# Kernel tuning notes

Hardware: AMD Instinct MI355X
Metric: run time of the kernel (lower is better)

Reference implementation:

```python
import jax, jax.numpy as jnp
import numpy as np

B, N, DH = 8, 2048, 512
EPS = 1e-5


def _layer_norm(x, g, b):
    m = x.mean(-1, keepdims=True)
    v = ((x - m) ** 2).mean(-1, keepdims=True)
    return (x - m) * jax.lax.rsqrt(v + EPS) * g + b


def setup_inputs() -> dict:
    key = jax.random.key(0)
    ks = jax.random.split(key, 20)
    s = 1.0 / np.sqrt(DH)
    sf = 1.0 / np.sqrt(2 * DH)
    return {
        "H": jax.random.normal(ks[0], (B, N, DH), jnp.float32),
        "adj": jax.random.uniform(ks[1], (B, N, N), jnp.float32),
        "hop_emb": jax.random.normal(ks[2], (N, DH), jnp.float32),
        "Wq": jax.random.normal(ks[3], (DH, DH), jnp.float32) * s,
        "bq": jnp.zeros((DH,), jnp.float32),
        "Wk": jax.random.normal(ks[4], (DH, DH), jnp.float32) * s,
        "bk": jnp.zeros((DH,), jnp.float32),
        "Wv": jax.random.normal(ks[5], (DH, DH), jnp.float32) * s,
        "bv": jnp.zeros((DH,), jnp.float32),
        "W1": jax.random.normal(ks[6], (DH, 2 * DH), jnp.float32) * s,
        "b1": jnp.zeros((2 * DH,), jnp.float32),
        "W2": jax.random.normal(ks[7], (2 * DH, DH), jnp.float32) * sf,
        "b2": jnp.zeros((DH,), jnp.float32),
        "g1": jnp.ones((DH,), jnp.float32),
        "be1": jnp.zeros((DH,), jnp.float32),
        "g2": jnp.ones((DH,), jnp.float32),
        "be2": jnp.zeros((DH,), jnp.float32),
    }


def reference(H, adj, hop_emb, Wq, bq, Wk, bk, Wv, bv, W1, b1, W2, b2, g1, be1, g2, be2):
    Q = H @ Wq + bq                                     # [B,N,DH]
    K = H @ Wk + bk
    V = H @ Wv + bv
    scores = jnp.einsum("bid,bjd->bij", Q, K) / np.sqrt(DH).astype(np.float32)
    # (adj[...,None] * hop_emb).mean(-1) == adj * hop_emb.mean(-1)[j]
    hop_effect = adj * hop_emb.mean(-1)[None, None, :]  # [B,N,N]
    attn = jax.nn.softmax(scores * hop_effect, axis=-1)
    attn_out = jnp.einsum("bij,bjd->bid", attn, V)
    x = _layer_norm(attn_out + H, g1, be1)
    ffn = jax.nn.relu(x @ W1 + b1) @ W2 + b2
    return _layer_norm(ffn + x, g2, be2)
```

## Files before the change

kernel.cpp:

```cpp
#include <hip/hip_runtime.h>

typedef unsigned short u16;
typedef __bf16 bf16x8 __attribute__((ext_vector_type(8)));
typedef float f32x4 __attribute__((ext_vector_type(4)));

#define SEQN 2048
#define DHID 512

static __device__ __forceinline__ float bf2f(u16 u) {
    union { unsigned int i; float f; } c; c.i = ((unsigned int)u) << 16; return c.f;
}
static __device__ __forceinline__ u16 f2bf(float f) {
    union { float f; unsigned int i; } c; c.f = f;
    unsigned int x = c.i;
    return (u16)((x + 0x7fffu + ((x >> 16) & 1u)) >> 16);
}

static __device__ __forceinline__ void gld_lds16(const u16* g, u16* l) {
    __builtin_amdgcn_global_load_lds(
        (__attribute__((address_space(1))) void*)(g),
        (__attribute__((address_space(3))) void*)(l), 16, 0, 0);
}

__global__ __launch_bounds__(256) void cvt_kernel(const float* __restrict__ src,
                                                  u16* __restrict__ dst, int n) {
    int i = (blockIdx.x * 256 + threadIdx.x) * 8;
    if (i >= n) return;
    float4 a = *(const float4*)(src + i);
    float4 b = *(const float4*)(src + i + 4);
    union { uint4 u; u16 s[8]; } o;
    o.s[0] = f2bf(a.x); o.s[1] = f2bf(a.y); o.s[2] = f2bf(a.z); o.s[3] = f2bf(a.w);
    o.s[4] = f2bf(b.x); o.s[5] = f2bf(b.y); o.s[6] = f2bf(b.z); o.s[7] = f2bf(b.w);
    *(uint4*)(dst + i) = o.u;
}

__global__ __launch_bounds__(256) void cvt_t_kernel(const float* __restrict__ src,
                                                    u16* __restrict__ dst, int K, int N) {
    int idx = blockIdx.x * 256 + threadIdx.x;
    if (idx >= K * N) return;
    int n = idx / K, k = idx - n * K;
    dst[idx] = f2bf(src[(size_t)k * N + n]);
}

__global__ void hmean_kernel(const float* __restrict__ hop, float* __restrict__ hm) {
    int j = blockIdx.x, t = threadIdx.x;
    const float* p = hop + (size_t)j * DHID + t * 8;
    float4 a = *(const float4*)p;
    float4 b = *(const float4*)(p + 4);
    float s = a.x + a.y + a.z + a.w + b.x + b.y + b.z + b.w;
#pragma unroll
    for (int m = 1; m < 64; m <<= 1) s += __shfl_xor(s, m);
    if (t == 0) hm[j] = s * (1.0f / (float)DHID);
}

enum { EPI_BIAS = 0, EPI_RELU = 1, EPI_PLAIN = 3, EPI_BIAS_T = 4, EPI_QKV = 5 };

template <int EPI>
__global__ __launch_bounds__(256) void gemm_bt(
    const u16* __restrict__ A, const u16* __restrict__ Bt, u16* __restrict__ C,
    const float* __restrict__ bias,
    int K, int lda, int ldb, int ldc,
    u16* __restrict__ Qo, u16* __restrict__ Ko, u16* __restrict__ Vto,
    const float* __restrict__ bq_, const float* __restrict__ bk_,
    const float* __restrict__ bv_)
{
    __shared__ u16 As[128 * 32];
    __shared__ u16 Bs[128 * 32];

    const int tid = threadIdx.x;
    const u16* Ab = A;
    const u16* Bb = Bt;

    const int bm0 = blockIdx.y * 128, bn0 = blockIdx.x * 128;
    const int wid = tid >> 6, lane = tid & 63, quad = lane >> 4, l16 = lane & 15;
    const int wm = (wid >> 1) * 64, wn = (wid & 1) * 64;
    const int srow = lane >> 2;
    const int skof = (lane & 3) * 8;

    f32x4 acc[4][4];
#pragma unroll
    for (int i = 0; i < 4; ++i)
#pragma unroll
        for (int j = 0; j < 4; ++j) acc[i][j] = (f32x4){0.f, 0.f, 0.f, 0.f};

    for (int k0 = 0; k0 < K; k0 += 32) {
#pragma unroll
        for (int it = 0; it < 2; ++it) {
            int c = wid * 2 + it;
            gld_lds16(Ab + (size_t)(bm0 + c * 16 + srow) * lda + k0 + skof,
                      &As[c * 512]);
        }
#pragma unroll
        for (int it = 0; it < 2; ++it) {
            int c = wid * 2 + it;
            gld_lds16(Bb + (size_t)(bn0 + c * 16 + srow) * ldb + k0 + skof,
                      &Bs[c * 512]);
        }
        __syncthreads();

        bf16x8 af[4], bfr[4];
#pragma unroll
        for (int i = 0; i < 4; ++i)
            af[i] = *(const bf16x8*)&As[(wm + i * 16 + l16) * 32 + quad * 8];
#pragma unroll
        for (int j = 0; j < 4; ++j)
            bfr[j] = *(const bf16x8*)&Bs[(wn + j * 16 + l16) * 32 + quad * 8];
#pragma unroll
        for (int i = 0; i < 4; ++i)
#pragma unroll
            for (int j = 0; j < 4; ++j)
                acc[i][j] = __builtin_amdgcn_mfma_f32_16x16x32_bf16(af[i], bfr[j], acc[i][j], 0, 0, 0);
        __syncthreads();
    }

#pragma unroll
    for (int i = 0; i < 4; ++i) {
#pragma unroll
        for (int j = 0; j < 4; ++j) {
            const int gn = bn0 + wn + j * 16 + l16;
            const int gm0 = bm0 + wm + i * 16 + quad * 4;
            if constexpr (EPI == EPI_BIAS || EPI == EPI_RELU) {
                const float b = bias[gn];
#pragma unroll
                for (int r = 0; r < 4; ++r) {
                    float v = acc[i][j][r] + b;
                    if constexpr (EPI == EPI_RELU) v = fmaxf(v, 0.f);
                    C[(size_t)(gm0 + r) * ldc + gn] = f2bf(v);
                }
            } else if constexpr (EPI == EPI_BIAS_T) {
                const float b = bias[gn];
                const int bb = gm0 >> 11, n = gm0 & 2047;
                ushort4 o;
                o.x = f2bf(acc[i][j][0] + b);
                o.y = f2bf(acc[i][j][1] + b);
                o.z = f2bf(acc[i][j][2] + b);
                o.w = f2bf(acc[i][j][3] + b);
                *(ushort4*)&C[((size_t)bb * 512 + gn) * 2048 + n] = o;
            } else if constexpr (EPI == EPI_QKV) {
                const int sel = gn >> 9;
                const int n = gn & 511;
                if (sel == 0) {
                    const float b = bq_[n];
#pragma unroll
                    for (int r = 0; r < 4; ++r)
                        Qo[(size_t)(gm0 + r) * DHID + n] = f2bf(acc[i][j][r] + b);
                } else if (sel == 1) {
                    const float b = bk_[n];
#pragma unroll
                    for (int r = 0; r < 4; ++r)
                        Ko[(size_t)(gm0 + r) * DHID + n] = f2bf(acc[i][j][r] + b);
                } else {
                    const float b = bv_[n];
                    const int bb = gm0 >> 11, nn2 = gm0 & 2047;
                    ushort4 o;
                    o.x = f2bf(acc[i][j][0] + b);
                    o.y = f2bf(acc[i][j][1] + b);
                    o.z = f2bf(acc[i][j][2] + b);
                    o.w = f2bf(acc[i][j][3] + b);
                    *(ushort4*)&Vto[((size_t)bb * 512 + n) * 2048 + nn2] = o;
                }
            } else {
#pragma unroll
                for (int r = 0; r < 4; ++r)
                    C[(size_t)(gm0 + r) * ldc + gn] = f2bf(acc[i][j][r]);
            }
        }
    }
}

__global__ __launch_bounds__(256, 2) void attn_kernel(
    const u16* __restrict__ Q, const u16* __restrict__ K, const u16* __restrict__ Vt,
    const float* __restrict__ adj, const float* __restrict__ hm,
    u16* __restrict__ AO)
{
    extern __shared__ u16 lds[];
    u16* Ks = lds;
    u16* Vs = lds + 16384;

    const int tid = threadIdx.x, wid = tid >> 6, lane = tid & 63;
    const int quad = lane >> 4, l16 = lane & 15;
    const int b = blockIdx.x;
    const int q0 = blockIdx.y * 32 + (wid >> 1) * 16;
    const int D0 = (wid & 1) * 256;
    const int srow = lane >> 2, sko = (lane & 3) * 8;

    const u16* Qg = Q + (size_t)b * SEQN * DHID;
    const u16* Kg = K + (size_t)b * SEQN * DHID;
    const u16* Vg = Vt + (size_t)b * DHID * SEQN;
    const float* adjg = adj + (size_t)b * SEQN * SEQN;
    u16* AOg = AO + (size_t)b * SEQN * DHID;
    u16* Plds = lds + wid * 640;

    const float scale = 0.044194173824159216f;

    bf16x8 qf[16];
#pragma unroll
    for (int ds = 0; ds < 16; ++ds)
        qf[ds] = *(const bf16x8*)(Qg + (size_t)(q0 + l16) * DHID + ds * 32 + quad * 8);

    f32x4 oacc[16];
#pragma unroll
    for (int dt = 0; dt < 16; ++dt) oacc[dt] = (f32x4){0.f, 0.f, 0.f, 0.f};
    float lsum[4] = {0.f, 0.f, 0.f, 0.f};

    for (int kt = 0; kt < 64; ++kt) {
        const int kv0 = kt * 32;

#pragma unroll
        for (int i = 0; i < 8; ++i) {
            int id = wid * 8 + i;
            int ds = id >> 1, c = id & 1;
            gld_lds16(Kg + (size_t)(kv0 + c * 16 + srow) * DHID + ds * 32 + sko,
                      &Ks[ds * 1024 + c * 512]);
        }
        __syncthreads();

#pragma unroll
        for (int i = 0; i < 8; ++i) {
            int id = wid * 8 + i;
            gld_lds16(Vg + (size_t)(id * 16 + srow) * SEQN + kv0 + sko,
                      &Vs[id * 512]);
        }

        float hv0 = hm[kv0 + l16] * scale;
        float hv1 = hm[kv0 + 16 + l16] * scale;
        float av[8];
        const float* arow = adjg + (size_t)(q0 + quad * 4) * SEQN + kv0;
#pragma unroll
        for (int r = 0; r < 4; ++r) {
            av[r]     = arow[(size_t)r * SEQN + l16];
            av[4 + r] = arow[(size_t)r * SEQN + 16 + l16];
        }

        f32x4 s0a = {0.f,0.f,0.f,0.f}, s0b = {0.f,0.f,0.f,0.f};
        f32x4 s1a = {0.f,0.f,0.f,0.f}, s1b = {0.f,0.f,0.f,0.f};
#pragma unroll
        for (int ds = 0; ds < 16; ds += 2) {
            bf16x8 k00 = *(const bf16x8*)&Ks[ds * 1024 + l16 * 32 + quad * 8];
            bf16x8 k01 = *(const bf16x8*)&Ks[ds * 1024 + 512 + l16 * 32 + quad * 8];
            s0a = __builtin_amdgcn_mfma_f32_16x16x32_bf16(qf[ds], k00, s0a, 0, 0, 0);
            s1a = __builtin_amdgcn_mfma_f32_16x16x32_bf16(qf[ds], k01, s1a, 0, 0, 0);
            bf16x8 k10 = *(const bf16x8*)&Ks[(ds + 1) * 1024 + l16 * 32 + quad * 8];
            bf16x8 k11 = *(const bf16x8*)&Ks[(ds + 1) * 1024 + 512 + l16 * 32 + quad * 8];
            s0b = __builtin_amdgcn_mfma_f32_16x16x32_bf16(qf[ds + 1], k10, s0b, 0, 0, 0);
            s1b = __builtin_amdgcn_mfma_f32_16x16x32_bf16(qf[ds + 1], k11, s1b, 0, 0, 0);
        }
        f32x4 s0 = s0a + s0b, s1 = s1a + s1b;
        __syncthreads();

#pragma unroll
        for (int r = 0; r < 4; ++r) {
            float p0 = __expf(s0[r] * av[r] * hv0);
            float p1 = __expf(s1[r] * av[4 + r] * hv1);
            lsum[r] += p0 + p1;
            Plds[(quad * 4 + r) * 40 + l16] = f2bf(p0);
            Plds[(quad * 4 + r) * 40 + 16 + l16] = f2bf(p1);
        }
        asm volatile("s_waitcnt lgkmcnt(0)" ::: "memory");

        bf16x8 pf = *(const bf16x8*)&Plds[l16 * 40 + quad * 8];
#pragma unroll
        for (int dt = 0; dt < 16; ++dt) {
            bf16x8 vf = *(const bf16x8*)&Vs[(D0 + dt * 16 + l16) * 32 + quad * 8];
            oacc[dt] = __builtin_amdgcn_mfma_f32_16x16x32_bf16(pf, vf, oacc[dt], 0, 0, 0);
        }
        __syncthreads();
    }

#pragma unroll
    for (int r = 0; r < 4; ++r) {
#pragma unroll
        for (int m = 1; m < 16; m <<= 1) lsum[r] += __shfl_xor(lsum[r], m);
        lsum[r] = 1.f / lsum[r];
    }
#pragma unroll
    for (int dt = 0; dt < 16; ++dt) {
#pragma unroll
        for (int r = 0; r < 4; ++r) {
            AOg[(size_t)(q0 + quad * 4 + r) * DHID + D0 + dt * 16 + l16] =
                f2bf(oacc[dt][r] * lsum[r]);
        }
    }
}

__global__ __launch_bounds__(256) void ln_hf32_kernel(
    const u16* __restrict__ a, const float* __restrict__ Hf,
    const float* __restrict__ g, const float* __restrict__ be,
    u16* __restrict__ out)
{
    size_t row = blockIdx.x;
    int t = threadIdx.x, wid = t >> 6, lane = t & 63;
    unsigned int va = *(const unsigned int*)(a + row * (size_t)DHID + t * 2);
    float2 h = *(const float2*)(Hf + row * (size_t)DHID + t * 2);
    float x0 = bf2f((u16)(va & 0xffff)) + h.x;
    float x1 = bf2f((u16)(va >> 16)) + h.y;
    float s = x0 + x1, sq = x0 * x0 + x1 * x1;
#pragma unroll
    for (int m = 1; m < 64; m <<= 1) { s += __shfl_xor(s, m); sq += __shfl_xor(sq, m); }
    __shared__ float rs[4], rq[4];
    if (lane == 0) { rs[wid] = s; rq[wid] = sq; }
    __syncthreads();
    s = rs[0] + rs[1] + rs[2] + rs[3];
    sq = rq[0] + rq[1] + rq[2] + rq[3];
    float mean = s * (1.f / (float)DHID);
    float var = sq * (1.f / (float)DHID) - mean * mean;
    float rstd = rsqrtf(var + 1e-5f);
    float2 vg = *(const float2*)(g + t * 2);
    float2 vbe = *(const float2*)(be + t * 2);
    float y0 = (x0 - mean) * rstd * vg.x + vbe.x;
    float y1 = (x1 - mean) * rstd * vg.y + vbe.y;
    unsigned int o = (unsigned int)f2bf(y0) | ((unsigned int)f2bf(y1) << 16);
    *(unsigned int*)(out + row * (size_t)DHID + t * 2) = o;
}

__global__ __launch_bounds__(256) void ln_kernel_f32out(
    const u16* __restrict__ a, const u16* __restrict__ bp,
    const float* __restrict__ g, const float* __restrict__ be,
    float* __restrict__ out)
{
    size_t row = blockIdx.x;
    int t = threadIdx.x, wid = t >> 6, lane = t & 63;
    unsigned int va = *(const unsigned int*)(a + row * (size_t)DHID + t * 2);
    unsigned int vb = *(const unsigned int*)(bp + row * (size_t)DHID + t * 2);
    float x0 = bf2f((u16)(va & 0xffff)) + bf2f((u16)(vb & 0xffff));
    float x1 = bf2f((u16)(va >> 16)) + bf2f((u16)(vb >> 16));
    float s = x0 + x1, sq = x0 * x0 + x1 * x1;
#pragma unroll
    for (int m = 1; m < 64; m <<= 1) { s += __shfl_xor(s, m); sq += __shfl_xor(sq, m); }
    __shared__ float rs[4], rq[4];
    if (lane == 0) { rs[wid] = s; rq[wid] = sq; }
    __syncthreads();
    s = rs[0] + rs[1] + rs[2] + rs[3];
    sq = rq[0] + rq[1] + rq[2] + rq[3];
    float mean = s * (1.f / (float)DHID);
    float var = sq * (1.f / (float)DHID) - mean * mean;
    float rstd = rsqrtf(var + 1e-5f);
    float2 vg = *(const float2*)(g + t * 2);
    float2 vbe = *(const float2*)(be + t * 2);
    float y0 = (x0 - mean) * rstd * vg.x + vbe.x;
    float y1 = (x1 - mean) * rstd * vg.y + vbe.y;
    *(float2*)(out + row * (size_t)DHID + t * 2) = make_float2(y0, y1);
}

extern "C" void kernel_launch(void* const* d_in, const int* in_sizes, int n_in,
                              void* d_out, int out_size, void* d_ws, size_t ws_size,
                              hipStream_t stream) {
    const float* H   = (const float*)d_in[0];
    const float* adj = (const float*)d_in[1];
    const float* hop = (const float*)d_in[2];
    const float* Wq  = (const float*)d_in[3];
    const float* bq  = (const float*)d_in[4];
    const float* Wk  = (const float*)d_in[5];
    const float* bk  = (const float*)d_in[6];
    const float* Wv  = (const float*)d_in[7];
    const float* bv  = (const float*)d_in[8];
    const float* W1  = (const float*)d_in[9];
    const float* b1  = (const float*)d_in[10];
    const float* W2  = (const float*)d_in[11];
    const float* b2  = (const float*)d_in[12];
    const float* g1  = (const float*)d_in[13];
    const float* be1 = (const float*)d_in[14];
    const float* g2  = (const float*)d_in[15];
    const float* be2 = (const float*)d_in[16];

    const size_t MiB = 1ull << 20;
    char* w = (char*)d_ws;
    float* hm   = (float*)w;
    u16* Hb    = (u16*)(w + 1 * MiB);
    u16* Wqkvt = (u16*)(w + 17 * MiB);
    u16* W1t   = (u16*)(w + 18 * MiB + 512 * 1024);
    u16* W2t   = (u16*)(w + 19 * MiB + 512 * 1024);
    u16* Q     = (u16*)(w + 21 * MiB);
    u16* Kb    = (u16*)(w + 37 * MiB);
    u16* Vt    = (u16*)(w + 53 * MiB);
    u16* AO    = (u16*)(w + 69 * MiB);
    u16* HID   = (u16*)(w + 85 * MiB);
    u16* X   = Kb;
    u16* F2  = Vt;

    const int BN = 8, N = SEQN, D = DHID;

    cvt_kernel<<<(BN * N * D) / (8 * 256), 256, 0, stream>>>(H, Hb, BN * N * D);
    cvt_t_kernel<<<(D * D + 255) / 256, 256, 0, stream>>>(Wq, Wqkvt, D, D);
    cvt_t_kernel<<<(D * D + 255) / 256, 256, 0, stream>>>(Wk, Wqkvt + D * D, D, D);
    cvt_t_kernel<<<(D * D + 255) / 256, 256, 0, stream>>>(Wv, Wqkvt + 2 * D * D, D, D);
    cvt_t_kernel<<<(D * 2 * D + 255) / 256, 256, 0, stream>>>(W1, W1t, D, 2 * D);
    cvt_t_kernel<<<(2 * D * D + 255) / 256, 256, 0, stream>>>(W2, W2t, 2 * D, D);

    hmean_kernel<<<N, 64, 0, stream>>>(hop, hm);

    gemm_bt<EPI_QKV><<<dim3(12, 128, 1), 256, 0, stream>>>(
        Hb, Wqkvt, nullptr, nullptr, D, D, D, 0, Q, Kb, Vt, bq, bk, bv);

    attn_kernel<<<dim3(8, 64), 256, 65536, stream>>>(Q, Kb, Vt, adj, hm, AO);

    ln_hf32_kernel<<<BN * N, 256, 0, stream>>>(AO, H, g1, be1, X);

    gemm_bt<EPI_RELU><<<dim3(8, 128, 1), 256, 0, stream>>>(
        X, W1t, HID, b1, D, D, D, 2 * D, nullptr, nullptr, nullptr, nullptr, nullptr, nullptr);

    gemm_bt<EPI_BIAS><<<dim3(4, 128, 1), 256, 0, stream>>>(
        HID, W2t, F2, b2, 2 * D, 2 * D, 2 * D, D, nullptr, nullptr, nullptr, nullptr, nullptr, nullptr);

    ln_kernel_f32out<<<BN * N, 256, 0, stream>>>(F2, X, g2, be2, (float*)d_out);
}
```

Baseline: 562.1 us.

## Double-buffer K tiles in LDS and load V fragments directly from global

The attention kernel now double-buffers the K tile in LDS, prefetching the next tile along with the next adj/hop values while the current QK^T MFMAs run. V is no longer staged through LDS; each wave reads its V fragments straight from global memory into registers. The P scratch reuses the current K buffer, which cuts one barrier per iteration. The cost is uncoalesced, strided global reads of V (eight rows of 16 bytes) and more register pressure. A race on the reused K buffer is also possible.

```diff
diff --git a/kernel.cpp b/kernel.cpp
--- a/kernel.cpp
+++ b/kernel.cpp
@@ -174,9 +174,6 @@
     u16* __restrict__ AO)
 {
     extern __shared__ u16 lds[];
-    u16* Ks = lds;
-    u16* Vs = lds + 16384;
-
     const int tid = threadIdx.x, wid = tid >> 6, lane = tid & 63;
     const int quad = lane >> 4, l16 = lane & 15;
     const int b = blockIdx.x;
@@ -186,10 +183,10 @@
 
     const u16* Qg = Q + (size_t)b * SEQN * DHID;
     const u16* Kg = K + (size_t)b * SEQN * DHID;
-    const u16* Vg = Vt + (size_t)b * DHID * SEQN;
+    const u16* Vg = Vt + (size_t)b * DHID * SEQN + (size_t)D0 * SEQN;
     const float* adjg = adj + (size_t)b * SEQN * SEQN;
     u16* AOg = AO + (size_t)b * SEQN * DHID;
-    u16* Plds = lds + wid * 640;
+    const float* arow = adjg + (size_t)(q0 + quad * 4) * SEQN;
 
     const float scale = 0.044194173824159216f;
 
@@ -203,51 +200,73 @@
     for (int dt = 0; dt < 16; ++dt) oacc[dt] = (f32x4){0.f, 0.f, 0.f, 0.f};
     float lsum[4] = {0.f, 0.f, 0.f, 0.f};
 
+    u16* ksCur = lds;
+    u16* ksNxt = lds + 16384;
+
+#pragma unroll
+    for (int i = 0; i < 8; ++i) {
+        int id = wid * 8 + i, ds = id >> 1, c = id & 1;
+        gld_lds16(Kg + (size_t)(c * 16 + srow) * DHID + ds * 32 + sko,
+                  &ksCur[ds * 1024 + c * 512]);
+    }
+    float av[8];
+#pragma unroll
+    for (int r = 0; r < 4; ++r) {
+        av[r]     = arow[(size_t)r * SEQN + l16];
+        av[4 + r] = arow[(size_t)r * SEQN + 16 + l16];
+    }
+    float hv0 = hm[l16] * scale;
+    float hv1 = hm[16 + l16] * scale;
+
     for (int kt = 0; kt < 64; ++kt) {
         const int kv0 = kt * 32;
-
-#pragma unroll
-        for (int i = 0; i < 8; ++i) {
-            int id = wid * 8 + i;
-            int ds = id >> 1, c = id & 1;
-            gld_lds16(Kg + (size_t)(kv0 + c * 16 + srow) * DHID + ds * 32 + sko,
-                      &Ks[ds * 1024 + c * 512]);
-        }
         __syncthreads();
 
-#pragma unroll
-        for (int i = 0; i < 8; ++i) {
-            int id = wid * 8 + i;
-            gld_lds16(Vg + (size_t)(id * 16 + srow) * SEQN + kv0 + sko,
-                      &Vs[id * 512]);
-        }
-
-        float hv0 = hm[kv0 + l16] * scale;
-        float hv1 = hm[kv0 + 16 + l16] * scale;
-        float av[8];
-        const float* arow = adjg + (size_t)(q0 + quad * 4) * SEQN + kv0;
-#pragma unroll
-        for (int r = 0; r < 4; ++r) {
-            av[r]     = arow[(size_t)r * SEQN + l16];
-            av[4 + r] = arow[(size_t)r * SEQN + 16 + l16];
+        if (kt < 63) {
+#pragma unroll
+            for (int i = 0; i < 8; ++i) {
+                int id = wid * 8 + i, ds = id >> 1, c = id & 1;
+                gld_lds16(Kg + (size_t)(kv0 + 32 + c * 16 + srow) * DHID + ds * 32 + sko,
+                          &ksNxt[ds * 1024 + c * 512]);
+            }
+        }
+        float avn[8] = {0.f, 0.f, 0.f, 0.f, 0.f, 0.f, 0.f, 0.f};
+        float hv0n = 0.f, hv1n = 0.f;
+        if (kt < 63) {
+#pragma unroll
+            for (int r = 0; r < 4; ++r) {
+                avn[r]     = arow[(size_t)r * SEQN + kv0 + 32 + l16];
+                avn[4 + r] = arow[(size_t)r * SEQN + kv0 + 48 + l16];
+            }
+            hv0n = hm[kv0 + 32 + l16] * scale;
+            hv1n = hm[kv0 + 48 + l16] * scale;
         }
 
         f32x4 s0a = {0.f,0.f,0.f,0.f}, s0b = {0.f,0.f,0.f,0.f};
         f32x4 s1a = {0.f,0.f,0.f,0.f}, s1b = {0.f,0.f,0.f,0.f};
 #pragma unroll
         for (int ds = 0; ds < 16; ds += 2) {
-            bf16x8 k00 = *(const bf16x8*)&Ks[ds * 1024 + l16 * 32 + quad * 8];
-            bf16x8 k01 = *(const bf16x8*)&Ks[ds * 1024 + 512 + l16 * 32 + quad * 8];
+            bf16x8 k00 = *(const bf16x8*)&ksCur[ds * 1024 + l16 * 32 + quad * 8];
+            bf16x8 k01 = *(const bf16x8*)&ksCur[ds * 1024 + 512 + l16 * 32 + quad * 8];
             s0a = __builtin_amdgcn_mfma_f32_16x16x32_bf16(qf[ds], k00, s0a, 0, 0, 0);
             s1a = __builtin_amdgcn_mfma_f32_16x16x32_bf16(qf[ds], k01, s1a, 0, 0, 0);
-            bf16x8 k10 = *(const bf16x8*)&Ks[(ds + 1) * 1024 + l16 * 32 + quad * 8];
-            bf16x8 k11 = *(const bf16x8*)&Ks[(ds + 1) * 1024 + 512 + l16 * 32 + quad * 8];
+            bf16x8 k10 = *(const bf16x8*)&ksCur[(ds + 1) * 1024 + l16 * 32 + quad * 8];
+            bf16x8 k11 = *(const bf16x8*)&ksCur[(ds + 1) * 1024 + 512 + l16 * 32 + quad * 8];
             s0b = __builtin_amdgcn_mfma_f32_16x16x32_bf16(qf[ds + 1], k10, s0b, 0, 0, 0);
             s1b = __builtin_amdgcn_mfma_f32_16x16x32_bf16(qf[ds + 1], k11, s1b, 0, 0, 0);
         }
         f32x4 s0 = s0a + s0b, s1 = s1a + s1b;
-        __syncthreads();
-
+
+        bf16x8 vfr[8];
+#pragma unroll
+        for (int dt = 0; dt < 8; ++dt)
+            vfr[dt] = *(const bf16x8*)(Vg + (size_t)(dt * 16 + l16) * SEQN + kv0 + quad * 8);
+
+        asm volatile("s_waitcnt lgkmcnt(0)" ::: "memory");
+        __builtin_amdgcn_s_barrier();
+        __builtin_amdgcn_sched_barrier(0);
+
+        u16* Plds = ksCur + wid * 640;
 #pragma unroll
         for (int r = 0; r < 4; ++r) {
             float p0 = __expf(s0[r] * av[r] * hv0);
@@ -257,14 +276,23 @@
             Plds[(quad * 4 + r) * 40 + 16 + l16] = f2bf(p1);
         }
         asm volatile("s_waitcnt lgkmcnt(0)" ::: "memory");
-
         bf16x8 pf = *(const bf16x8*)&Plds[l16 * 40 + quad * 8];
-#pragma unroll
-        for (int dt = 0; dt < 16; ++dt) {
-            bf16x8 vf = *(const bf16x8*)&Vs[(D0 + dt * 16 + l16) * 32 + quad * 8];
+
+#pragma unroll
+        for (int dt = 0; dt < 8; ++dt)
+            oacc[dt] = __builtin_amdgcn_mfma_f32_16x16x32_bf16(pf, vfr[dt], oacc[dt], 0, 0, 0);
+#pragma unroll
+        for (int dt = 8; dt < 16; ++dt) {
+            bf16x8 vf = *(const bf16x8*)(Vg + (size_t)(dt * 16 + l16) * SEQN + kv0 + quad * 8);
             oacc[dt] = __builtin_amdgcn_mfma_f32_16x16x32_bf16(pf, vf, oacc[dt], 0, 0, 0);
         }
-        __syncthreads();
+
+        if (kt < 63) {
+#pragma unroll
+            for (int r = 0; r < 8; ++r) av[r] = avn[r];
+            hv0 = hv0n; hv1 = hv1n;
+        }
+        u16* t = ksCur; ksCur = ksNxt; ksNxt = t;
     }
 
 #pragma unroll
```

Result: slower. 714.9 us (+27.2%).
